# Kernel tuning notes

Measured on AMD Instinct MI355X. Metric: run time of the kernel, lower is better.

## Reference

```python
import jax, jax.numpy as jnp
import numpy as np

B, N, T, D = 256, 12, 20, 512
EPS_A = 1e-6          # adjacency row-sum epsilon (matches torch code)
EPS_BN = 1e-5         # BatchNorm2d default eps
DIST_THRESH = 150.0   # pixel distance threshold for graph edges


def setup_inputs() -> dict:
    key = jax.random.key(0)
    ks = jax.random.split(key, 16)
    person_features = jax.random.normal(ks[0], (B, N, T, D), dtype=jnp.float32)
    # bboxes: (x, y, w, h) in pixel coordinates of a 1280x720 frame
    bboxes = jax.random.uniform(ks[1], (B, N, 4), dtype=jnp.float32) \
             * jnp.array([1280.0, 720.0, 120.0, 200.0], dtype=jnp.float32)
    inp = {"person_features": person_features, "bboxes": bboxes}
    # STGCN layer params: 1x1 conv == per-node linear [D_out, D_in], plus BN affine + running stats
    for li in (1, 2):
        k = jax.random.split(ks[1 + li], 6)
        inp[f"W{li}"] = jax.random.normal(k[0], (D, D), dtype=jnp.float32) * (1.0 / np.sqrt(D))
        inp[f"b{li}"] = jax.random.normal(k[1], (D,), dtype=jnp.float32) * 0.01
        inp[f"g{li}"] = jnp.ones((D,), dtype=jnp.float32) + 0.1 * jax.random.normal(k[2], (D,), dtype=jnp.float32)
        inp[f"beta{li}"] = 0.1 * jax.random.normal(k[3], (D,), dtype=jnp.float32)
        inp[f"m{li}"] = 0.1 * jax.random.normal(k[4], (D,), dtype=jnp.float32)
        inp[f"v{li}"] = 0.5 + jax.random.uniform(k[5], (D,), dtype=jnp.float32)
    return inp


def _stgcn(x, A_norm, W, b, g, beta, m, v):
    # x: [B, N, C]; A_norm: [B, N, N] row-normalized adjacency
    # torch: out[c, j] = sum_n x[n, c] * A_norm[n, j]
    xg = jnp.einsum('bnc,bnj->bjc', x, A_norm)           # graph aggregation
    y = xg @ W.T + b                                      # 1x1 conv over channels
    y = g * (y - m) * jax.lax.rsqrt(v + EPS_BN) + beta    # BatchNorm2d (inference)
    return jax.nn.relu(y)


def reference(person_features, bboxes, W1, b1, g1, beta1, m1, v1,
              W2, b2, g2, beta2, m2, v2):
    # box centers: (x + w/2, y + h/2)  -> [B, N, 2]
    centers = jnp.stack([bboxes[..., 0] + bboxes[..., 2] * 0.5,
                         bboxes[..., 1] + bboxes[..., 3] * 0.5], axis=-1)
    # squared pairwise distance (threshold on d^2 avoids sqrt-at-zero); diag d=0<150 -> 1,
    # identical to off-diag threshold + added identity in the torch code.
    diff = centers[:, :, None, :] - centers[:, None, :, :]   # [B, N, N, 2]
    d2 = jnp.sum(diff * diff, axis=-1)                       # [B, N, N]
    A = (d2 < DIST_THRESH * DIST_THRESH).astype(jnp.float32)
    A_norm = A / (jnp.sum(A, axis=-1, keepdims=True) + EPS_A)

    x = person_features[:, :, -1, :]                         # last timestep [B, N, D]
    x = _stgcn(x, A_norm, W1, b1, g1, beta1, m1, v1)
    x = _stgcn(x, A_norm, W2, b2, g2, beta2, m2, v2)
    # write enhanced features back into the last timestep
    return person_features.at[:, :, -1, :].set(x)
```

## Files before the change

kernel.cpp:

```cpp
#include <hip/hip_runtime.h>

#define BB 256
#define NP 12
#define TT 20
#define DD 512
#define EPS_A 1e-6f
#define EPS_BN 1e-5f
#define THR2 (150.0f * 150.0f)
#define MROWS (BB * NP)
#define PITCH 40

typedef __attribute__((ext_vector_type(8))) short shortx8;
typedef __attribute__((ext_vector_type(4))) float floatx4;

static __device__ __forceinline__ ushort f2bf(float f) {
    unsigned x = __float_as_uint(f);
    return (ushort)((x + 0x7fffu + ((x >> 16) & 1u)) >> 16);
}

static __device__ __forceinline__ void copy_body(int cb, int ncb, long lo, long hi,
                                                 const float4* __restrict__ src,
                                                 float4* __restrict__ dst, bool skip) {
    long stride = (long)ncb * 256;
    for (long g = lo + (long)cb * 256 + threadIdx.x; g < hi; g += stride) {
        if (skip) {
            int row = (int)(g >> 7);
            if (row % TT == TT - 1) continue;
        }
        dst[g] = src[g];
    }
}

__global__ __launch_bounds__(256) void k1_prep(
    const float* __restrict__ pf, const float* __restrict__ bboxes,
    const float* __restrict__ W1, const float* __restrict__ W2,
    const float* __restrict__ b1, const float* __restrict__ g1,
    const float* __restrict__ beta1, const float* __restrict__ m1, const float* __restrict__ v1,
    const float* __restrict__ b2, const float* __restrict__ g2,
    const float* __restrict__ beta2, const float* __restrict__ m2, const float* __restrict__ v2,
    float* __restrict__ atg, float* __restrict__ s1, float* __restrict__ t1,
    float* __restrict__ s2, float* __restrict__ t2,
    ushort* __restrict__ wb1, ushort* __restrict__ wb2, ushort* __restrict__ xg1,
    const float4* __restrict__ csrc, float4* __restrict__ cdst) {
    int bid = blockIdx.x, t = threadIdx.x;
    if (bid < BB) {
        int b = bid;
        __shared__ float cx[NP], cy[NP], Ash[NP][NP], rinv[NP], at[NP][NP];
        if (t < NP) {
            const float* p = bboxes + (b * NP + t) * 4;
            cx[t] = p[0] + 0.5f * p[2];
            cy[t] = p[1] + 0.5f * p[3];
        }
        __syncthreads();
        if (t < NP * NP) {
            int n = t / NP, k = t % NP;
            float dx = cx[n] - cx[k], dy = cy[n] - cy[k];
            Ash[n][k] = (dx * dx + dy * dy < THR2) ? 1.f : 0.f;
        }
        __syncthreads();
        if (t < NP) {
            float s = 0.f;
            #pragma unroll
            for (int k = 0; k < NP; k++) s += Ash[t][k];
            rinv[t] = 1.f / (s + EPS_A);
        }
        __syncthreads();
        if (t < NP * NP) {
            int j = t / NP, n = t % NP;
            float val = Ash[n][j] * rinv[n];
            at[j][n] = val;
            atg[b * NP * NP + t] = val;
        }
        __syncthreads();
        for (int c = t; c < DD; c += 256) {
            float xv[NP];
            #pragma unroll
            for (int n = 0; n < NP; n++)
                xv[n] = pf[((long)((b * NP + n) * TT + TT - 1)) * DD + c];
            #pragma unroll
            for (int j = 0; j < NP; j++) {
                float a = 0.f;
                #pragma unroll
                for (int n = 0; n < NP; n++) a += at[j][n] * xv[n];
                xg1[(long)(b * NP + j) * DD + c] = f2bf(a);
            }
        }
    } else if (bid < 320) {
        int idx = (bid - 256) * 256 + t;
        for (int i = idx; i < 131072; i += 16384) {
            float4 f = (i < 65536) ? ((const float4*)W1)[i] : ((const float4*)W2)[i - 65536];
            ushort4 u;
            u.x = f2bf(f.x); u.y = f2bf(f.y); u.z = f2bf(f.z); u.w = f2bf(f.w);
            if (i < 65536) *(ushort4*)(wb1 + (long)i * 4) = u;
            else           *(ushort4*)(wb2 + (long)(i - 65536) * 4) = u;
        }
    } else if (bid == 320) {
        for (int d = t; d < DD; d += 256) {
            float sa = g1[d] * rsqrtf(v1[d] + EPS_BN);
            s1[d] = sa; t1[d] = (b1[d] - m1[d]) * sa + beta1[d];
            float sb = g2[d] * rsqrtf(v2[d] + EPS_BN);
            s2[d] = sb; t2[d] = (b2[d] - m2[d]) * sb + beta2[d];
        }
    } else {
        copy_body(bid - 321, 256, 0L, 524288L, csrc, cdst, false);
    }
}

template <int LAYER>
static __device__ void gemm_body(int bid, int t,
                                 const ushort* __restrict__ xg, const ushort* __restrict__ wb,
                                 const float* __restrict__ sv, const float* __restrict__ tv,
                                 float* __restrict__ out) {
    __shared__ __align__(16) ushort Alds[64 * PITCH];
    __shared__ __align__(16) ushort Blds[64 * PITCH];
    int m0 = (bid >> 3) * 64;
    int n0 = (bid & 7) * 64;
    int wave = t >> 6, lane = t & 63;
    int quad = lane >> 4, mrow = lane & 15;
    int r = t >> 2, seg = t & 3;

    floatx4 acc[4] = {{0, 0, 0, 0}, {0, 0, 0, 0}, {0, 0, 0, 0}, {0, 0, 0, 0}};

    const uint4* gA = (const uint4*)(xg + (long)(m0 + r) * DD + seg * 8);
    const uint4* gB = (const uint4*)(wb + (long)(n0 + r) * DD + seg * 8);
    uint4* lA = (uint4*)&Alds[r * PITCH + seg * 8];
    uint4* lB = (uint4*)&Blds[r * PITCH + seg * 8];
    const ushort* ra = &Alds[(wave * 16 + mrow) * PITCH + quad * 8];
    const ushort* rb = &Blds[mrow * PITCH + quad * 8];

    for (int kc = 0; kc < DD; kc += 32) {
        uint4 av = gA[kc >> 3];
        uint4 bv = gB[kc >> 3];
        __syncthreads();
        *lA = av;
        *lB = bv;
        __syncthreads();
        shortx8 af = *(const shortx8*)ra;
        #pragma unroll
        for (int nt = 0; nt < 4; nt++) {
            shortx8 bf = *(const shortx8*)(rb + nt * 16 * PITCH);
            acc[nt] = __builtin_amdgcn_mfma_f32_16x16x32_bf16(af, bf, acc[nt], 0, 0, 0);
        }
    }

    #pragma unroll
    for (int nt = 0; nt < 4; nt++) {
        int d = n0 + nt * 16 + mrow;
        float s = sv[d], tt = tv[d];
        #pragma unroll
        for (int v = 0; v < 4; v++) {
            int m = m0 + wave * 16 + quad * 4 + v;
            float val = fmaxf(acc[nt][v] * s + tt, 0.f);
            if (LAYER == 1) out[(long)m * DD + d] = val;
            else            out[((long)m * TT + (TT - 1)) * DD + d] = val;
        }
    }
}

template <int LAYER>
__global__ __launch_bounds__(256) void k_gemm(
    const ushort* __restrict__ xg, const ushort* __restrict__ wb,
    const float* __restrict__ sv, const float* __restrict__ tv, float* __restrict__ out,
    const float4* __restrict__ csrc, float4* __restrict__ cdst,
    long clo, long chi, int skip) {
    int bid = blockIdx.x;
    if (bid < 384) gemm_body<LAYER>(bid, threadIdx.x, xg, wb, sv, tv, out);
    else copy_body(bid - 384, 832, clo, chi, csrc, cdst, skip != 0);
}

__global__ __launch_bounds__(256) void k3_mix2(
    const float* __restrict__ y1v, const float* __restrict__ atg, ushort* __restrict__ xg2,
    const float4* __restrict__ csrc, float4* __restrict__ cdst) {
    int bid = blockIdx.x, t = threadIdx.x;
    if (bid < BB) {
        __shared__ float at[NP * NP];
        if (t < NP * NP) at[t] = atg[bid * NP * NP + t];
        __syncthreads();
        for (int c = t; c < DD; c += 256) {
            float xv[NP];
            #pragma unroll
            for (int n = 0; n < NP; n++) xv[n] = y1v[(long)(bid * NP + n) * DD + c];
            #pragma unroll
            for (int j = 0; j < NP; j++) {
                float a = 0.f;
                #pragma unroll
                for (int n = 0; n < NP; n++) a += at[j * NP + n] * xv[n];
                xg2[(long)(bid * NP + j) * DD + c] = f2bf(a);
            }
        }
    } else {
        copy_body(bid - 256, 256, 3932160L, 4456448L, csrc, cdst, false);
    }
}

extern "C" void kernel_launch(void* const* d_in, const int* in_sizes, int n_in,
                              void* d_out, int out_size, void* d_ws, size_t ws_size,
                              hipStream_t stream) {
    const float* pf = (const float*)d_in[0];
    const float* bboxes = (const float*)d_in[1];
    const float* W1 = (const float*)d_in[2];
    const float* b1 = (const float*)d_in[3];
    const float* g1 = (const float*)d_in[4];
    const float* beta1 = (const float*)d_in[5];
    const float* m1 = (const float*)d_in[6];
    const float* v1 = (const float*)d_in[7];
    const float* W2 = (const float*)d_in[8];
    const float* b2 = (const float*)d_in[9];
    const float* g2 = (const float*)d_in[10];
    const float* beta2 = (const float*)d_in[11];
    const float* m2 = (const float*)d_in[12];
    const float* v2 = (const float*)d_in[13];
    float* out = (float*)d_out;

    float* ws = (float*)d_ws;
    float* atg = ws;
    float* s1 = ws + 36864;
    float* t1v = s1 + 512;
    float* s2 = t1v + 512;
    float* t2v = s2 + 512;
    ushort* wb1 = (ushort*)(t2v + 512);
    ushort* wb2 = wb1 + 262144;
    ushort* xg1 = wb2 + 262144;
    ushort* xg2 = xg1 + (long)MROWS * DD;
    float* y1v = (float*)(xg2 + (long)MROWS * DD);

    const float4* csrc = (const float4*)pf;
    float4* cdst = (float4*)out;

    k1_prep<<<577, 256, 0, stream>>>(pf, bboxes, W1, W2, b1, g1, beta1, m1, v1,
                                     b2, g2, beta2, m2, v2, atg, s1, t1v, s2, t2v,
                                     wb1, wb2, xg1, csrc, cdst);
    k_gemm<1><<<1216, 256, 0, stream>>>(xg1, wb1, s1, t1v, y1v, csrc, cdst,
                                        524288L, 3932160L, 0);
    k3_mix2<<<512, 256, 0, stream>>>(y1v, atg, xg2, csrc, cdst);
    k_gemm<2><<<1216, 256, 0, stream>>>(xg2, wb2, s2, t2v, out, csrc, cdst,
                                        4456448L, 7864320L, 1);
}
```

Measured before the change: 264.6 us.

## Fuse adjacency, both graph mixes and both GEMM layers into one per-batch kernel

Replaces the four-kernel pipeline with a weight-prep kernel plus a single fused kernel. In the fused kernel each of 256 blocks handles one batch: it builds the adjacency, mixes features into LDS, runs both 12x512x512 bf16 MFMA GEMMs with weights read directly from global memory, and keeps the intermediate layer in LDS. The bulk passthrough copy is spread over extra blocks in the same launch. This removes the global round-trips for xg1, y1 and xg2 and two launch boundaries. In exchange, 16-row tiles waste a quarter of the MFMA work on padding, and every block re-reads both full weight matrices from L2.

```diff
diff --git a/kernel.cpp b/kernel.cpp
--- a/kernel.cpp
+++ b/kernel.cpp
@@ -7,8 +7,10 @@
 #define EPS_A 1e-6f
 #define EPS_BN 1e-5f
 #define THR2 (150.0f * 150.0f)
-#define MROWS (BB * NP)
-#define PITCH 40
+#define APITCH 520
+#define COPY_TOTAL 7864320L
+#define C0 491520L
+#define NCPY 1792
 
 typedef __attribute__((ext_vector_type(8))) short shortx8;
 typedef __attribute__((ext_vector_type(4))) float floatx4;
@@ -20,73 +22,27 @@
 
 static __device__ __forceinline__ void copy_body(int cb, int ncb, long lo, long hi,
                                                  const float4* __restrict__ src,
-                                                 float4* __restrict__ dst, bool skip) {
+                                                 float4* __restrict__ dst) {
     long stride = (long)ncb * 256;
     for (long g = lo + (long)cb * 256 + threadIdx.x; g < hi; g += stride) {
-        if (skip) {
-            int row = (int)(g >> 7);
-            if (row % TT == TT - 1) continue;
-        }
+        int row = (int)(g >> 7);
+        if (row % TT == TT - 1) continue;
         dst[g] = src[g];
     }
 }
 
-__global__ __launch_bounds__(256) void k1_prep(
-    const float* __restrict__ pf, const float* __restrict__ bboxes,
+__global__ __launch_bounds__(256) void k_prep(
     const float* __restrict__ W1, const float* __restrict__ W2,
     const float* __restrict__ b1, const float* __restrict__ g1,
     const float* __restrict__ beta1, const float* __restrict__ m1, const float* __restrict__ v1,
     const float* __restrict__ b2, const float* __restrict__ g2,
     const float* __restrict__ beta2, const float* __restrict__ m2, const float* __restrict__ v2,
-    float* __restrict__ atg, float* __restrict__ s1, float* __restrict__ t1,
-    float* __restrict__ s2, float* __restrict__ t2,
-    ushort* __restrict__ wb1, ushort* __restrict__ wb2, ushort* __restrict__ xg1,
+    float* __restrict__ s1, float* __restrict__ t1, float* __restrict__ s2, float* __restrict__ t2,
+    ushort* __restrict__ wb1, ushort* __restrict__ wb2,
     const float4* __restrict__ csrc, float4* __restrict__ cdst) {
     int bid = blockIdx.x, t = threadIdx.x;
-    if (bid < BB) {
-        int b = bid;
-        __shared__ float cx[NP], cy[NP], Ash[NP][NP], rinv[NP], at[NP][NP];
-        if (t < NP) {
-            const float* p = bboxes + (b * NP + t) * 4;
-            cx[t] = p[0] + 0.5f * p[2];
-            cy[t] = p[1] + 0.5f * p[3];
-        }
-        __syncthreads();
-        if (t < NP * NP) {
-            int n = t / NP, k = t % NP;
-            float dx = cx[n] - cx[k], dy = cy[n] - cy[k];
-            Ash[n][k] = (dx * dx + dy * dy < THR2) ? 1.f : 0.f;
-        }
-        __syncthreads();
-        if (t < NP) {
-            float s = 0.f;
-            #pragma unroll
-            for (int k = 0; k < NP; k++) s += Ash[t][k];
-            rinv[t] = 1.f / (s + EPS_A);
-        }
-        __syncthreads();
-        if (t < NP * NP) {
-            int j = t / NP, n = t % NP;
-            float val = Ash[n][j] * rinv[n];
-            at[j][n] = val;
-            atg[b * NP * NP + t] = val;
-        }
-        __syncthreads();
-        for (int c = t; c < DD; c += 256) {
-            float xv[NP];
-            #pragma unroll
-            for (int n = 0; n < NP; n++)
-                xv[n] = pf[((long)((b * NP + n) * TT + TT - 1)) * DD + c];
-            #pragma unroll
-            for (int j = 0; j < NP; j++) {
-                float a = 0.f;
-                #pragma unroll
-                for (int n = 0; n < NP; n++) a += at[j][n] * xv[n];
-                xg1[(long)(b * NP + j) * DD + c] = f2bf(a);
-            }
-        }
-    } else if (bid < 320) {
-        int idx = (bid - 256) * 256 + t;
+    if (bid < 64) {
+        int idx = bid * 256 + t;
         for (int i = idx; i < 131072; i += 16384) {
             float4 f = (i < 65536) ? ((const float4*)W1)[i] : ((const float4*)W2)[i - 65536];
             ushort4 u;
@@ -94,7 +50,7 @@
             if (i < 65536) *(ushort4*)(wb1 + (long)i * 4) = u;
             else           *(ushort4*)(wb2 + (long)(i - 65536) * 4) = u;
         }
-    } else if (bid == 320) {
+    } else if (bid == 64) {
         for (int d = t; d < DD; d += 256) {
             float sa = g1[d] * rsqrtf(v1[d] + EPS_BN);
             s1[d] = sa; t1[d] = (b1[d] - m1[d]) * sa + beta1[d];
@@ -102,95 +58,130 @@
             s2[d] = sb; t2[d] = (b2[d] - m2[d]) * sb + beta2[d];
         }
     } else {
-        copy_body(bid - 321, 256, 0L, 524288L, csrc, cdst, false);
+        copy_body(bid - 65, 191, 0L, C0, csrc, cdst);
     }
 }
 
 template <int LAYER>
-static __device__ void gemm_body(int bid, int t,
-                                 const ushort* __restrict__ xg, const ushort* __restrict__ wb,
-                                 const float* __restrict__ sv, const float* __restrict__ tv,
-                                 float* __restrict__ out) {
-    __shared__ __align__(16) ushort Alds[64 * PITCH];
-    __shared__ __align__(16) ushort Blds[64 * PITCH];
-    int m0 = (bid >> 3) * 64;
-    int n0 = (bid & 7) * 64;
-    int wave = t >> 6, lane = t & 63;
-    int quad = lane >> 4, mrow = lane & 15;
-    int r = t >> 2, seg = t & 3;
-
-    floatx4 acc[4] = {{0, 0, 0, 0}, {0, 0, 0, 0}, {0, 0, 0, 0}, {0, 0, 0, 0}};
-
-    const uint4* gA = (const uint4*)(xg + (long)(m0 + r) * DD + seg * 8);
-    const uint4* gB = (const uint4*)(wb + (long)(n0 + r) * DD + seg * 8);
-    uint4* lA = (uint4*)&Alds[r * PITCH + seg * 8];
-    uint4* lB = (uint4*)&Blds[r * PITCH + seg * 8];
-    const ushort* ra = &Alds[(wave * 16 + mrow) * PITCH + quad * 8];
-    const ushort* rb = &Blds[mrow * PITCH + quad * 8];
-
+static __device__ __forceinline__ void gemm16(
+    int wave, int lane, int b,
+    const ushort (*__restrict__ xgl)[APITCH], float (*__restrict__ y1l)[DD],
+    const ushort* __restrict__ wb, const float* __restrict__ sv, const float* __restrict__ tv,
+    float* __restrict__ outp) {
+    int mrow = lane & 15, quad = lane >> 4;
+    floatx4 acc[8];
+    #pragma unroll
+    for (int nt = 0; nt < 8; nt++) acc[nt] = (floatx4){0.f, 0.f, 0.f, 0.f};
+
+    const ushort* wbase = wb + ((long)(wave * 128 + mrow)) * DD + quad * 8;
+    #pragma unroll 2
     for (int kc = 0; kc < DD; kc += 32) {
-        uint4 av = gA[kc >> 3];
-        uint4 bv = gB[kc >> 3];
-        __syncthreads();
-        *lA = av;
-        *lB = bv;
-        __syncthreads();
-        shortx8 af = *(const shortx8*)ra;
-        #pragma unroll
-        for (int nt = 0; nt < 4; nt++) {
-            shortx8 bf = *(const shortx8*)(rb + nt * 16 * PITCH);
+        shortx8 af = *(const shortx8*)&xgl[mrow][kc + quad * 8];
+        #pragma unroll
+        for (int nt = 0; nt < 8; nt++) {
+            shortx8 bf = *(const shortx8*)(wbase + nt * 16 * DD + kc);
             acc[nt] = __builtin_amdgcn_mfma_f32_16x16x32_bf16(af, bf, acc[nt], 0, 0, 0);
         }
     }
 
     #pragma unroll
-    for (int nt = 0; nt < 4; nt++) {
-        int d = n0 + nt * 16 + mrow;
+    for (int nt = 0; nt < 8; nt++) {
+        int d = wave * 128 + nt * 16 + mrow;
         float s = sv[d], tt = tv[d];
         #pragma unroll
         for (int v = 0; v < 4; v++) {
-            int m = m0 + wave * 16 + quad * 4 + v;
+            int m = quad * 4 + v;
             float val = fmaxf(acc[nt][v] * s + tt, 0.f);
-            if (LAYER == 1) out[(long)m * DD + d] = val;
-            else            out[((long)m * TT + (TT - 1)) * DD + d] = val;
-        }
-    }
-}
-
-template <int LAYER>
-__global__ __launch_bounds__(256) void k_gemm(
-    const ushort* __restrict__ xg, const ushort* __restrict__ wb,
-    const float* __restrict__ sv, const float* __restrict__ tv, float* __restrict__ out,
-    const float4* __restrict__ csrc, float4* __restrict__ cdst,
-    long clo, long chi, int skip) {
-    int bid = blockIdx.x;
-    if (bid < 384) gemm_body<LAYER>(bid, threadIdx.x, xg, wb, sv, tv, out);
-    else copy_body(bid - 384, 832, clo, chi, csrc, cdst, skip != 0);
-}
-
-__global__ __launch_bounds__(256) void k3_mix2(
-    const float* __restrict__ y1v, const float* __restrict__ atg, ushort* __restrict__ xg2,
+            if (m < NP) {
+                if (LAYER == 1) y1l[m][d] = val;
+                else outp[((long)(b * NP + m) * TT + TT - 1) * DD + d] = val;
+            }
+        }
+    }
+}
+
+__global__ __launch_bounds__(256) void k_fused(
+    const float* __restrict__ pf, const float* __restrict__ bboxes,
+    const ushort* __restrict__ wb1, const ushort* __restrict__ wb2,
+    const float* __restrict__ s1, const float* __restrict__ t1,
+    const float* __restrict__ s2, const float* __restrict__ t2,
+    float* __restrict__ out,
     const float4* __restrict__ csrc, float4* __restrict__ cdst) {
+    __shared__ float cx[NP], cy[NP], Ash[NP][NP], rinv[NP], at[NP][NP];
+    __shared__ __align__(16) ushort xgl[16][APITCH];
+    __shared__ float y1l[NP][DD];
+
     int bid = blockIdx.x, t = threadIdx.x;
-    if (bid < BB) {
-        __shared__ float at[NP * NP];
-        if (t < NP * NP) at[t] = atg[bid * NP * NP + t];
-        __syncthreads();
-        for (int c = t; c < DD; c += 256) {
-            float xv[NP];
+    if (bid >= BB) {
+        copy_body(bid - BB, NCPY, C0, COPY_TOTAL, csrc, cdst);
+        return;
+    }
+
+    int b = bid;
+    int lane = t & 63, wave = t >> 6;
+
+    if (t < NP) {
+        const float* p = bboxes + (b * NP + t) * 4;
+        cx[t] = p[0] + 0.5f * p[2];
+        cy[t] = p[1] + 0.5f * p[3];
+    }
+    {
+        uint* xz = (uint*)&xgl[NP][0];
+        for (int i = t; i < 4 * APITCH / 2; i += 256) xz[i] = 0;
+    }
+    __syncthreads();
+    if (t < NP * NP) {
+        int n = t / NP, k = t % NP;
+        float dx = cx[n] - cx[k], dy = cy[n] - cy[k];
+        Ash[n][k] = (dx * dx + dy * dy < THR2) ? 1.f : 0.f;
+    }
+    __syncthreads();
+    if (t < NP) {
+        float s = 0.f;
+        #pragma unroll
+        for (int k = 0; k < NP; k++) s += Ash[t][k];
+        rinv[t] = 1.f / (s + EPS_A);
+    }
+    __syncthreads();
+    if (t < NP * NP) {
+        int j = t / NP, n = t % NP;
+        at[j][n] = Ash[n][j] * rinv[n];
+    }
+    __syncthreads();
+
+    for (int c = t; c < DD; c += 256) {
+        float xv[NP];
+        #pragma unroll
+        for (int n = 0; n < NP; n++)
+            xv[n] = pf[((long)((b * NP + n) * TT + TT - 1)) * DD + c];
+        #pragma unroll
+        for (int j = 0; j < NP; j++) {
+            float a = 0.f;
             #pragma unroll
-            for (int n = 0; n < NP; n++) xv[n] = y1v[(long)(bid * NP + n) * DD + c];
+            for (int n = 0; n < NP; n++) a += at[j][n] * xv[n];
+            xgl[j][c] = f2bf(a);
+        }
+    }
+    __syncthreads();
+
+    gemm16<1>(wave, lane, b, xgl, y1l, wb1, s1, t1, nullptr);
+    __syncthreads();
+
+    for (int c = t; c < DD; c += 256) {
+        float xv[NP];
+        #pragma unroll
+        for (int n = 0; n < NP; n++) xv[n] = y1l[n][c];
+        #pragma unroll
+        for (int j = 0; j < NP; j++) {
+            float a = 0.f;
             #pragma unroll
-            for (int j = 0; j < NP; j++) {
-                float a = 0.f;
-                #pragma unroll
-                for (int n = 0; n < NP; n++) a += at[j * NP + n] * xv[n];
-                xg2[(long)(bid * NP + j) * DD + c] = f2bf(a);
-            }
-        }
-    } else {
-        copy_body(bid - 256, 256, 3932160L, 4456448L, csrc, cdst, false);
-    }
+            for (int n = 0; n < NP; n++) a += at[j][n] * xv[n];
+            xgl[j][c] = f2bf(a);
+        }
+    }
+    __syncthreads();
+
+    gemm16<2>(wave, lane, b, xgl, y1l, wb2, s2, t2, out);
 }
 
 extern "C" void kernel_launch(void* const* d_in, const int* in_sizes, int n_in,
@@ -213,26 +204,19 @@
     float* out = (float*)d_out;
 
     float* ws = (float*)d_ws;
-    float* atg = ws;
-    float* s1 = ws + 36864;
-    float* t1v = s1 + 512;
-    float* s2 = t1v + 512;
-    float* t2v = s2 + 512;
-    ushort* wb1 = (ushort*)(t2v + 512);
+    float* s1 = ws;
+    float* t1v = ws + 512;
+    float* s2 = ws + 1024;
+    float* t2v = ws + 1536;
+    ushort* wb1 = (ushort*)(ws + 2048);
     ushort* wb2 = wb1 + 262144;
-    ushort* xg1 = wb2 + 262144;
-    ushort* xg2 = xg1 + (long)MROWS * DD;
-    float* y1v = (float*)(xg2 + (long)MROWS * DD);
 
     const float4* csrc = (const float4*)pf;
     float4* cdst = (float4*)out;
 
-    k1_prep<<<577, 256, 0, stream>>>(pf, bboxes, W1, W2, b1, g1, beta1, m1, v1,
-                                     b2, g2, beta2, m2, v2, atg, s1, t1v, s2, t2v,
-                                     wb1, wb2, xg1, csrc, cdst);
-    k_gemm<1><<<1216, 256, 0, stream>>>(xg1, wb1, s1, t1v, y1v, csrc, cdst,
-                                        524288L, 3932160L, 0);
-    k3_mix2<<<512, 256, 0, stream>>>(y1v, atg, xg2, csrc, cdst);
-    k_gemm<2><<<1216, 256, 0, stream>>>(xg2, wb2, s2, t2v, out, csrc, cdst,
-                                        4456448L, 7864320L, 1);
-}
+    k_prep<<<256, 256, 0, stream>>>(W1, W2, b1, g1, beta1, m1, v1,
+                                    b2, g2, beta2, m2, v2,
+                                    s1, t1v, s2, t2v, wb1, wb2, csrc, cdst);
+    k_fused<<<BB + NCPY, 256, 0, stream>>>(pf, bboxes, wb1, wb2,
+                                           s1, t1v, s2, t2v, out, csrc, cdst);
+}
```

Result: slower. 285.5 us (+7.9%).
